# Performance work log

Hardware: AMD Instinct MI355X
Metric: run time of the kernel (lower is better)

Reference implementation:

```python
import jax, jax.numpy as jnp
import numpy as np
import math

S, E, D, H = 2048, 1024, 64, 16  # seq, embedding_dim (=D*H), per-head d_model, heads


def setup_inputs() -> dict:
    ks = jax.random.split(jax.random.key(0), 14)
    u = lambda k, sh: jax.random.uniform(k, sh, dtype=jnp.float32)
    n = lambda k, sh, s=0.02: s * jax.random.normal(k, sh, dtype=jnp.float32)
    return {
        "x": jax.random.normal(ks[0], (S, E), dtype=jnp.float32),
        # nn.Parameter(torch.rand(d_model, embedding_dim))
        "Wk": u(ks[1], (D, E)),
        "Wq": u(ks[2], (D, E)),
        "Wv": u(ks[3], (D, E)),
        # per-head Linear(d_model, d_model): weight [out,in]=[D,D], bias [D]
        "hWk": n(ks[4], (H, D, D)), "hbk": n(ks[5], (H, D)),
        "hWv": n(ks[6], (H, D, D)), "hbv": n(ks[7], (H, D)),
        "hWq": n(ks[8], (H, D, D)), "hbq": n(ks[9], (H, D)),
        # last_linear: Linear(D*H, D*H)
        "Wo": n(ks[10], (E, E)), "bo": n(ks[11], (E,)),
        # LayerNorm(D*H)
        "gamma": jnp.ones((E,), jnp.float32),
        "beta": jnp.zeros((E,), jnp.float32),
    }


def reference(x, Wk, Wq, Wv, hWk, hbk, hWv, hbv, hWq, hbq, Wo, bo, gamma, beta):
    # shared projections: [S, E] @ [E, D] -> [S, D]
    K = x @ Wk.T
    Q = x @ Wq.T
    V = x @ Wv.T
    # per-head linears (torch Linear: y = x @ W.T + b), vectorized over heads
    Kh = jnp.einsum('sd,hed->hse', K, hWk) + hbk[:, None, :]  # [H, S, D]
    Vh = jnp.einsum('sd,hed->hse', V, hWv) + hbv[:, None, :]
    Qh = jnp.einsum('sd,hed->hse', Q, hWq) + hbq[:, None, :]
    # scaled dot product attention; scale uses sqrt(d_model)
    scores = jnp.einsum('hqd,hkd->hqk', Qh, Kh) / math.sqrt(D)  # [H, S, S]
    attn = jax.nn.softmax(scores, axis=-1)
    O = jnp.einsum('hqk,hkd->hqd', attn, Vh)  # [H, S, D]
    # concat heads along feature dim (head order) -> [S, H*D]
    cat = jnp.transpose(O, (1, 0, 2)).reshape(S, H * D)
    out = cat @ Wo.T + bo
    # residual + LayerNorm (eps 1e-5)
    y = out + x
    mu = jnp.mean(y, axis=-1, keepdims=True)
    var = jnp.mean(jnp.square(y - mu), axis=-1, keepdims=True)
    return (y - mu) * jax.lax.rsqrt(var + 1e-5) * gamma + beta
```

## Files before the change

kernel.cpp:

```cpp
#include <hip/hip_runtime.h>
#include <math.h>

#define S 2048
#define E 1024
#define D 64
#define H 16

using f16 = _Float16;
typedef _Float16 v8h __attribute__((ext_vector_type(8)));
typedef _Float16 v4h __attribute__((ext_vector_type(4)));
typedef float v4f __attribute__((ext_vector_type(4)));

__device__ __forceinline__ void glds16(const f16* g, f16* l) {
    __builtin_amdgcn_global_load_lds(
        (const __attribute__((address_space(1))) void*)g,
        (__attribute__((address_space(3))) void*)l, 16, 0, 0);
}

__global__ void x_convert(const float* __restrict__ x, f16* __restrict__ Xh) {
    const size_t i = (size_t)blockIdx.x * 256 + threadIdx.x;
    v4f w = ((const v4f*)x)[i];
    v4h h = {(f16)w[0], (f16)w[1], (f16)w[2], (f16)w[3]};
    ((v4h*)Xh)[i] = h;
}
__global__ void wo_convert(const float* __restrict__ Wo, f16* __restrict__ WoB) {
    const size_t i = (size_t)blockIdx.x * 256 + threadIdx.x;
    v4f w = ((const v4f*)Wo)[i];
    v4h h = {(f16)w[0], (f16)w[1], (f16)w[2], (f16)w[3]};
    ((v4h*)WoB)[i] = h;
}

__global__ void wprep(const float* __restrict__ hWk, const float* __restrict__ hWq,
                      const float* __restrict__ hWv,
                      const float* __restrict__ Wk, const float* __restrict__ Wq,
                      const float* __restrict__ Wv,
                      f16* __restrict__ Wc) {
    const int th = blockIdx.x;
    const int type = th >> 4, h = th & 15;
    const int e0 = blockIdx.y * 64;
    const float* hW = ((type == 0) ? hWk : (type == 1) ? hWq : hWv) + (size_t)h * D * D;
    const float* W  = (type == 0) ? Wk : (type == 1) ? Wq : Wv;
    const int t = threadIdx.x;

    __shared__ f16 Ah[64][72];
    __shared__ f16 Bt[64][72];

    {
        const int r16 = t >> 4, c4 = (t & 15) * 4;
#pragma unroll
        for (int rep = 0; rep < 4; ++rep) {
            const int row = rep * 16 + r16;
            v4f a = *(const v4f*)&hW[(size_t)row * D + c4];
#pragma unroll
            for (int j = 0; j < 4; ++j) Ah[row][c4 + j] = (f16)a[j];
            v4f w = *(const v4f*)&W[(size_t)row * E + e0 + c4];
#pragma unroll
            for (int j = 0; j < 4; ++j) Bt[c4 + j][row] = (f16)w[j];
        }
    }
    __syncthreads();

    const int wave = t >> 6, lane = t & 63;
    const int quad = lane >> 4, l16 = lane & 15;
    v4f acc[4] = {{0,0,0,0},{0,0,0,0},{0,0,0,0},{0,0,0,0}};
#pragma unroll
    for (int ks = 0; ks < 2; ++ks) {
        v8h af = *(const v8h*)&Ah[wave * 16 + l16][ks * 32 + quad * 8];
#pragma unroll
        for (int nt = 0; nt < 4; ++nt) {
            v8h bf = *(const v8h*)&Bt[nt * 16 + l16][ks * 32 + quad * 8];
            acc[nt] = __builtin_amdgcn_mfma_f32_16x16x32_f16(af, bf, acc[nt], 0, 0, 0);
        }
    }
#pragma unroll
    for (int r = 0; r < 4; ++r) {
        const int e2 = wave * 16 + quad * 4 + r;
#pragma unroll
        for (int nt = 0; nt < 4; ++nt)
            Wc[((size_t)th * D + e2) * E + e0 + nt * 16 + l16] = (f16)acc[nt][r];
    }
}

__global__ __launch_bounds__(256) void qkv_gemm(
        const f16* __restrict__ Xh, const f16* __restrict__ Wc,
        const float* __restrict__ hbk, const float* __restrict__ hbq,
        const float* __restrict__ hbv,
        f16* __restrict__ Kh, f16* __restrict__ Qh, f16* __restrict__ Vh) {
    const int m0 = blockIdx.x * 128;
    const int n0 = blockIdx.y * 64;
    const int type = n0 >> 10, h = (n0 >> 6) & 15;
    const float* hb = ((type == 0) ? hbk : (type == 1) ? hbq : hbv) + h * D;
    f16* outp = (type == 0) ? Kh : (type == 1) ? Qh : Vh;

    const int t = threadIdx.x;
    const int wave = t >> 6, lane = t & 63;
    const int quad = lane >> 4, l16 = lane & 15;
    const int wm = wave >> 1, wn = wave & 1;

    __shared__ f16 As[128 * 64];
    __shared__ f16 Bs[64 * 64];

    v4f acc[4][2] = {};

    const int lrow8 = lane >> 3, lg = lane & 7;

    for (int k0 = 0; k0 < E; k0 += 64) {
        __syncthreads();
#pragma unroll
        for (int jj = 0; jj < 4; ++jj) {
            const int j = wave * 4 + jj;
            const int row = j * 8 + lrow8;
            const int g = lg ^ (row & 7);
            glds16(Xh + (size_t)(m0 + row) * E + k0 + g * 8, &As[j * 512]);
        }
#pragma unroll
        for (int jj = 0; jj < 2; ++jj) {
            const int j = wave * 2 + jj;
            const int row = j * 8 + lrow8;
            const int g = lg ^ (row & 7);
            glds16(Wc + (size_t)(n0 + row) * E + k0 + g * 8, &Bs[j * 512]);
        }
        __syncthreads();

#pragma unroll
        for (int ks = 0; ks < 2; ++ks) {
            v8h a[4], b[2];
#pragma unroll
            for (int mt = 0; mt < 4; ++mt) {
                const int row = wm * 64 + mt * 16 + l16;
                a[mt] = *(const v8h*)&As[row * 64 + (((ks * 4 + quad) ^ (row & 7)) * 8)];
            }
#pragma unroll
            for (int nt = 0; nt < 2; ++nt) {
                const int row = wn * 32 + nt * 16 + l16;
                b[nt] = *(const v8h*)&Bs[row * 64 + (((ks * 4 + quad) ^ (row & 7)) * 8)];
            }
#pragma unroll
            for (int mt = 0; mt < 4; ++mt)
#pragma unroll
                for (int nt = 0; nt < 2; ++nt)
                    acc[mt][nt] = __builtin_amdgcn_mfma_f32_16x16x32_f16(a[mt], b[nt], acc[mt][nt], 0, 0, 0);
        }
    }

#pragma unroll
    for (int mt = 0; mt < 4; ++mt)
#pragma unroll
        for (int r = 0; r < 4; ++r) {
            const int s = m0 + wm * 64 + mt * 16 + quad * 4 + r;
#pragma unroll
            for (int nt = 0; nt < 2; ++nt) {
                const int d = wn * 32 + nt * 16 + l16;
                outp[((size_t)h * S + s) * D + d] = (f16)(acc[mt][nt][r] + hb[d]);
            }
        }
}

__global__ void v_transpose(const f16* __restrict__ Vh, f16* __restrict__ VhT) {
    const int h = blockIdx.x;
    const int s0 = blockIdx.y * 64;
    const int t = threadIdx.x;

    __shared__ f16 T[64][66];

    {
        const int r = t >> 2, c = (t & 3) * 16;
        v8h a = *(const v8h*)(Vh + ((size_t)h * S + s0 + r) * D + c);
        v8h b = *(const v8h*)(Vh + ((size_t)h * S + s0 + r) * D + c + 8);
#pragma unroll
        for (int j = 0; j < 8; ++j) { T[r][c + j] = a[j]; T[r][c + 8 + j] = b[j]; }
    }
    __syncthreads();
    {
        const int d = t >> 2, sc = (t & 3) * 16;
        v8h a, b;
#pragma unroll
        for (int j = 0; j < 8; ++j) { a[j] = T[sc + j][d]; b[j] = T[sc + 8 + j][d]; }
        f16* o = VhT + ((size_t)h * D + d) * S + s0 + sc;
        *(v8h*)o = a;
        *(v8h*)(o + 8) = b;
    }
}

#define TK2 64
#define NSPLIT 2
#define KSPAN (S / NSPLIT)
#define ITERS (KSPAN / TK2)
#define APAD 72

__global__ __launch_bounds__(256) void attn_mfma(
        const f16* __restrict__ Qh, const f16* __restrict__ Kh,
        const f16* __restrict__ VhT, f16* __restrict__ Opart,
        float* __restrict__ ml) {
    const int h = blockIdx.y;
    const int q0 = blockIdx.x * 64;
    const int sp = blockIdx.z;
    const int t = threadIdx.x;
    const int wave = t >> 6, lane = t & 63;
    const int quad = lane >> 4, l16 = lane & 15;

    __shared__ f16 Kt[TK2][APAD];
    __shared__ f16 Vt[D][APAD];
    __shared__ f16 Pt[4][16][APAD];
    __shared__ f16 Ot[64][APAD];

    const int qrow = q0 + wave * 16 + l16;
    v8h qf[2];
    {
        const v8h* qp = (const v8h*)(Qh + ((size_t)h * S + qrow) * D);
        qf[0] = qp[quad];
        qf[1] = qp[quad + 4];
    }

    v4f oc[4] = {};
    float m_run = -INFINITY, l_run = 0.f;
    const float scale = 0.125f * 1.44269504f;

    const int sr = t >> 2, scc = (t & 3) * 16;
    const int kb = sp * KSPAN;

    v8h kA, kB, vA, vB;
    {
        const f16* kg = Kh + ((size_t)h * S + kb + sr) * D + scc;
        kA = *(const v8h*)kg; kB = *(const v8h*)(kg + 8);
        const f16* vg = VhT + ((size_t)h * D + sr) * S + kb + scc;
        vA = *(const v8h*)vg; vB = *(const v8h*)(vg + 8);
    }

    for (int it = 0; it < ITERS; ++it) {
        __syncthreads();
        *(v8h*)&Kt[sr][scc] = kA;  *(v8h*)&Kt[sr][scc + 8] = kB;
        *(v8h*)&Vt[sr][scc] = vA;  *(v8h*)&Vt[sr][scc + 8] = vB;
        __syncthreads();

        if (it + 1 < ITERS) {
            const int nb = kb + (it + 1) * TK2;
            const f16* kg = Kh + ((size_t)h * S + nb + sr) * D + scc;
            kA = *(const v8h*)kg; kB = *(const v8h*)(kg + 8);
            const f16* vg = VhT + ((size_t)h * D + sr) * S + nb + scc;
            vA = *(const v8h*)vg; vB = *(const v8h*)(vg + 8);
        }

        v4f sc[4] = {};
#pragma unroll
        for (int ks = 0; ks < 2; ++ks) {
#pragma unroll
            for (int mt = 0; mt < 4; ++mt) {
                v8h kf = *(const v8h*)&Kt[mt * 16 + l16][ks * 32 + quad * 8];
                sc[mt] = __builtin_amdgcn_mfma_f32_16x16x32_f16(kf, qf[ks], sc[mt], 0, 0, 0);
            }
        }

        float v = sc[0][0];
#pragma unroll
        for (int mt = 0; mt < 4; ++mt)
#pragma unroll
            for (int r = 0; r < 4; ++r) v = fmaxf(v, sc[mt][r]);
        v = fmaxf(v, __shfl_xor(v, 16));
        v = fmaxf(v, __shfl_xor(v, 32));
        v *= scale;
        const float mnew = fmaxf(m_run, v);
        const float alpha = exp2f(m_run - mnew);
        m_run = mnew;

        float tsum = 0.f;
#pragma unroll
        for (int mt = 0; mt < 4; ++mt) {
            v4h ph;
#pragma unroll
            for (int r = 0; r < 4; ++r) {
                const float p = exp2f(fmaf(sc[mt][r], scale, -mnew));
                tsum += p;
                ph[r] = (f16)p;
            }
            *(v4h*)&Pt[wave][l16][mt * 16 + quad * 4] = ph;
        }
        tsum += __shfl_xor(tsum, 16);
        tsum += __shfl_xor(tsum, 32);
        l_run = l_run * alpha + tsum;
#pragma unroll
        for (int mt = 0; mt < 4; ++mt) oc[mt] *= alpha;

#pragma unroll
        for (int ks = 0; ks < 2; ++ks) {
            v8h pf = *(const v8h*)&Pt[wave][l16][ks * 32 + quad * 8];
#pragma unroll
            for (int mt = 0; mt < 4; ++mt) {
                v8h vf = *(const v8h*)&Vt[mt * 16 + l16][ks * 32 + quad * 8];
                oc[mt] = __builtin_amdgcn_mfma_f32_16x16x32_f16(vf, pf, oc[mt], 0, 0, 0);
            }
        }
    }

    const float invl = 1.f / l_run;
#pragma unroll
    for (int mt = 0; mt < 4; ++mt) {
        v4h oh;
#pragma unroll
        for (int r = 0; r < 4; ++r) oh[r] = (f16)(oc[mt][r] * invl);
        *(v4h*)&Ot[wave * 16 + l16][mt * 16 + quad * 4] = oh;
    }
    if (quad == 0) {
        float* mlp = ml + (((size_t)sp * H + h) * S + qrow) * 2;
        mlp[0] = m_run;
        mlp[1] = l_run;
    }
    __syncthreads();
    {
        const int q = t >> 2, dg = (t & 3) * 16;
        v8h o0 = *(const v8h*)&Ot[q][dg];
        v8h o1 = *(const v8h*)&Ot[q][dg + 8];
        f16* dst = Opart + (((size_t)sp * H + h) * S + q0 + q) * D + dg;
        *(v8h*)dst = o0;
        *(v8h*)(dst + 8) = o1;
    }
}

__global__ void attn_combine(const f16* __restrict__ Opart,
                             const float* __restrict__ ml,
                             f16* __restrict__ cat) {
    const int q = blockIdx.x;
    const int t = threadIdx.x;
#pragma unroll
    for (int i = 0; i < 4; ++i) {
        const int idx = i * 256 + t;
        const int h = idx >> 6, d = idx & 63;
        const size_t b0 = ((size_t)0 * H + h) * S + q;
        const size_t b1 = ((size_t)1 * H + h) * S + q;
        const float m0 = ml[b0 * 2], l0 = ml[b0 * 2 + 1];
        const float m1 = ml[b1 * 2], l1 = ml[b1 * 2 + 1];
        const float M = fmaxf(m0, m1);
        const float a0 = exp2f(m0 - M) * l0;
        const float a1 = exp2f(m1 - M) * l1;
        const float inv = 1.f / (a0 + a1);
        const float o = (a0 * (float)Opart[b0 * D + d] + a1 * (float)Opart[b1 * D + d]) * inv;
        cat[(size_t)q * E + h * D + d] = (f16)o;
    }
}

__global__ __launch_bounds__(256) void gemm_y(
        const f16* __restrict__ cat, const f16* __restrict__ WoB,
        const float* __restrict__ bo, const float* __restrict__ x,
        float* __restrict__ y) {
    const int m0 = blockIdx.x * 64;
    const int n0 = blockIdx.y * 64;
    const int t = threadIdx.x;
    const int wave = t >> 6, lane = t & 63;
    const int quad = lane >> 4, l16 = lane & 15;
    const int wm = wave >> 1, wn = wave & 1;

    __shared__ f16 As[64 * 64];
    __shared__ f16 Bs[64 * 64];

    v4f acc[2][2] = {};
    const int lrow8 = lane >> 3, lg = lane & 7;

    for (int k0 = 0; k0 < E; k0 += 64) {
        __syncthreads();
#pragma unroll
        for (int jj = 0; jj < 2; ++jj) {
            const int j = wave * 2 + jj;
            const int row = j * 8 + lrow8;
            const int g = lg ^ (row & 7);
            glds16(cat + (size_t)(m0 + row) * E + k0 + g * 8, &As[j * 512]);
            glds16(WoB + (size_t)(n0 + row) * E + k0 + g * 8, &Bs[j * 512]);
        }
        __syncthreads();

#pragma unroll
        for (int ks = 0; ks < 2; ++ks) {
            v8h a[2], b[2];
#pragma unroll
            for (int mt = 0; mt < 2; ++mt) {
                const int row = wm * 32 + mt * 16 + l16;
                a[mt] = *(const v8h*)&As[row * 64 + (((ks * 4 + quad) ^ (row & 7)) * 8)];
            }
#pragma unroll
            for (int nt = 0; nt < 2; ++nt) {
                const int row = wn * 32 + nt * 16 + l16;
                b[nt] = *(const v8h*)&Bs[row * 64 + (((ks * 4 + quad) ^ (row & 7)) * 8)];
            }
#pragma unroll
            for (int mt = 0; mt < 2; ++mt)
#pragma unroll
                for (int nt = 0; nt < 2; ++nt)
                    acc[mt][nt] = __builtin_amdgcn_mfma_f32_16x16x32_f16(a[mt], b[nt], acc[mt][nt], 0, 0, 0);
        }
    }

#pragma unroll
    for (int mt = 0; mt < 2; ++mt)
#pragma unroll
        for (int r = 0; r < 4; ++r) {
            const int m = m0 + wm * 32 + mt * 16 + quad * 4 + r;
#pragma unroll
            for (int nt = 0; nt < 2; ++nt) {
                const int e = n0 + wn * 32 + nt * 16 + l16;
                y[(size_t)m * E + e] = acc[mt][nt][r] + bo[e] + x[(size_t)m * E + e];
            }
        }
}

__global__ void ln(const float* __restrict__ y,
                   const float* __restrict__ gamma,
                   const float* __restrict__ beta,
                   float* __restrict__ out) {
    const int s = blockIdx.x;
    const int t = threadIdx.x;
    __shared__ float red[256];

    v4f yv = *(const v4f*)(y + (size_t)s * E + t * 4);
    float lsum = yv[0] + yv[1] + yv[2] + yv[3];
    red[t] = lsum;
    __syncthreads();
    for (int w = 128; w > 0; w >>= 1) {
        if (t < w) red[t] += red[t + w];
        __syncthreads();
    }
    const float mu = red[0] * (1.f / E);
    __syncthreads();

    float lv = 0.f;
#pragma unroll
    for (int i = 0; i < 4; ++i) { float dd = yv[i] - mu; lv += dd * dd; }
    red[t] = lv;
    __syncthreads();
    for (int w = 128; w > 0; w >>= 1) {
        if (t < w) red[t] += red[t + w];
        __syncthreads();
    }
    const float rstd = rsqrtf(red[0] * (1.f / E) + 1e-5f);

    v4f o;
#pragma unroll
    for (int i = 0; i < 4; ++i) {
        const int e = t * 4 + i;
        o[i] = (yv[i] - mu) * rstd * gamma[e] + beta[e];
    }
    *(v4f*)(out + (size_t)s * E + t * 4) = o;
}

extern "C" void kernel_launch(void* const* d_in, const int* in_sizes, int n_in,
                              void* d_out, int out_size, void* d_ws, size_t ws_size,
                              hipStream_t stream) {
    const float* x     = (const float*)d_in[0];
    const float* Wk    = (const float*)d_in[1];
    const float* Wq    = (const float*)d_in[2];
    const float* Wv    = (const float*)d_in[3];
    const float* hWk   = (const float*)d_in[4];
    const float* hbk   = (const float*)d_in[5];
    const float* hWv   = (const float*)d_in[6];
    const float* hbv   = (const float*)d_in[7];
    const float* hWq   = (const float*)d_in[8];
    const float* hbq   = (const float*)d_in[9];
    const float* Wo    = (const float*)d_in[10];
    const float* bo    = (const float*)d_in[11];
    const float* gamma = (const float*)d_in[12];
    const float* beta  = (const float*)d_in[13];
    float* out = (float*)d_out;

    char* base = (char*)d_ws;
    const size_t MB = 1u << 20;
    f16*   Xh    = (f16*)(base);
    f16*   Wc    = (f16*)(base + 4 * MB);
    f16*   Kh    = (f16*)(base + 12 * MB);
    f16*   Qh    = (f16*)(base + 16 * MB);
    f16*   Vh    = (f16*)(base + 20 * MB);
    f16*   VhT   = (f16*)(base);
    f16*   Opart = (f16*)(base + 4 * MB);
    f16*   cat   = (f16*)(base + 24 * MB);
    f16*   WoB   = (f16*)(base + 28 * MB);
    float* ml    = (float*)(base + 30 * MB);
    float* y     = (float*)(base);

    x_convert<<<(S * E / 4) / 256, 256, 0, stream>>>(x, Xh);
    wo_convert<<<(E * E / 4) / 256, 256, 0, stream>>>(Wo, WoB);
    wprep<<<dim3(3 * H, E / 64), 256, 0, stream>>>(hWk, hWq, hWv, Wk, Wq, Wv, Wc);
    qkv_gemm<<<dim3(S / 128, 3 * H * D / 64), 256, 0, stream>>>(Xh, Wc, hbk, hbq, hbv,
                                                                Kh, Qh, Vh);
    v_transpose<<<dim3(H, S / 64), 256, 0, stream>>>(Vh, VhT);
    attn_mfma<<<dim3(S / 64, H, NSPLIT), 256, 0, stream>>>(Qh, Kh, VhT, Opart, ml);
    attn_combine<<<S, 256, 0, stream>>>(Opart, ml, cat);
    gemm_y<<<dim3(S / 64, E / 64), 256, 0, stream>>>(cat, WoB, bo, x, y);
    ln<<<S, 256, 0, stream>>>(y, gamma, beta, out);
}
```

Baseline: 179.5 us.

## Rework attention: direct-to-LDS swizzled K/V loads, 4-way split, MFMA row sum

The attention kernel now loads K and V^T tiles straight into swizzled LDS with global_load_lds instead of staging them through registers. The key dimension is split 4 ways instead of 2, and launch bounds are raised to 5 blocks per CU. The softmax row sum is computed by an extra MFMA against a row of ones appended to V, and the exponentials use the hardware exp2 intrinsic with packed f16 conversion. The two conversion kernels are merged into one and workspace buffers are rearranged. The cost is the loss of register prefetch overlap and more partial outputs for the combine step to merge.

```diff
diff --git a/kernel.cpp b/kernel.cpp
--- a/kernel.cpp
+++ b/kernel.cpp
@@ -9,7 +9,10 @@
 using f16 = _Float16;
 typedef _Float16 v8h __attribute__((ext_vector_type(8)));
 typedef _Float16 v4h __attribute__((ext_vector_type(4)));
+typedef _Float16 v2h __attribute__((ext_vector_type(2)));
 typedef float v4f __attribute__((ext_vector_type(4)));
+
+__device__ __forceinline__ float fexp2(float x) { return __builtin_amdgcn_exp2f(x); }
 
 __device__ __forceinline__ void glds16(const f16* g, f16* l) {
     __builtin_amdgcn_global_load_lds(
@@ -17,17 +20,20 @@
         (__attribute__((address_space(3))) void*)l, 16, 0, 0);
 }
 
-__global__ void x_convert(const float* __restrict__ x, f16* __restrict__ Xh) {
+__global__ void convert_all(const float* __restrict__ x, const float* __restrict__ Wo,
+                            f16* __restrict__ Xh, f16* __restrict__ WoB) {
     const size_t i = (size_t)blockIdx.x * 256 + threadIdx.x;
-    v4f w = ((const v4f*)x)[i];
-    v4h h = {(f16)w[0], (f16)w[1], (f16)w[2], (f16)w[3]};
-    ((v4h*)Xh)[i] = h;
-}
-__global__ void wo_convert(const float* __restrict__ Wo, f16* __restrict__ WoB) {
-    const size_t i = (size_t)blockIdx.x * 256 + threadIdx.x;
-    v4f w = ((const v4f*)Wo)[i];
-    v4h h = {(f16)w[0], (f16)w[1], (f16)w[2], (f16)w[3]};
-    ((v4h*)WoB)[i] = h;
+    const size_t NX = (size_t)S * E / 4;
+    if (i < NX) {
+        v4f w = ((const v4f*)x)[i];
+        v4h h = {(f16)w[0], (f16)w[1], (f16)w[2], (f16)w[3]};
+        ((v4h*)Xh)[i] = h;
+    } else {
+        const size_t j = i - NX;
+        v4f w = ((const v4f*)Wo)[j];
+        v4h h = {(f16)w[0], (f16)w[1], (f16)w[2], (f16)w[3]};
+        ((v4h*)WoB)[j] = h;
+    }
 }
 
 __global__ void wprep(const float* __restrict__ hWk, const float* __restrict__ hWq,
@@ -101,7 +107,6 @@
     __shared__ f16 Bs[64 * 64];
 
     v4f acc[4][2] = {};
-
     const int lrow8 = lane >> 3, lg = lane & 7;
 
     for (int k0 = 0; k0 < E; k0 += 64) {
@@ -182,13 +187,12 @@
     }
 }
 
-#define TK2 64
-#define NSPLIT 2
+#define NSPLIT 4
 #define KSPAN (S / NSPLIT)
-#define ITERS (KSPAN / TK2)
-#define APAD 72
-
-__global__ __launch_bounds__(256) void attn_mfma(
+#define ITERS (KSPAN / 64)
+#define PPAD 72
+
+__global__ __launch_bounds__(256, 5) void attn_mfma(
         const f16* __restrict__ Qh, const f16* __restrict__ Kh,
         const f16* __restrict__ VhT, f16* __restrict__ Opart,
         float* __restrict__ ml) {
@@ -199,10 +203,14 @@
     const int wave = t >> 6, lane = t & 63;
     const int quad = lane >> 4, l16 = lane & 15;
 
-    __shared__ f16 Kt[TK2][APAD];
-    __shared__ f16 Vt[D][APAD];
-    __shared__ f16 Pt[4][16][APAD];
-    __shared__ f16 Ot[64][APAD];
+    __shared__ f16 Kt[64 * 64];
+    __shared__ f16 Vt[80 * 64];
+    __shared__ union { f16 P[4][16][PPAD]; f16 O[64][PPAD]; } PO;
+
+    {
+        v4h one = {(f16)1, (f16)1, (f16)1, (f16)1};
+        *(v4h*)&Vt[64 * 64 + t * 4] = one;
+    }
 
     const int qrow = q0 + wave * 16 + l16;
     v8h qf[2];
@@ -212,44 +220,34 @@
         qf[1] = qp[quad + 4];
     }
 
-    v4f oc[4] = {};
-    float m_run = -INFINITY, l_run = 0.f;
+    v4f oc[5] = {};
+    float m_run = -INFINITY;
     const float scale = 0.125f * 1.44269504f;
-
-    const int sr = t >> 2, scc = (t & 3) * 16;
     const int kb = sp * KSPAN;
-
-    v8h kA, kB, vA, vB;
-    {
-        const f16* kg = Kh + ((size_t)h * S + kb + sr) * D + scc;
-        kA = *(const v8h*)kg; kB = *(const v8h*)(kg + 8);
-        const f16* vg = VhT + ((size_t)h * D + sr) * S + kb + scc;
-        vA = *(const v8h*)vg; vB = *(const v8h*)(vg + 8);
-    }
+    const int srow = lane >> 3, sg = lane & 7;
 
     for (int it = 0; it < ITERS; ++it) {
         __syncthreads();
-        *(v8h*)&Kt[sr][scc] = kA;  *(v8h*)&Kt[sr][scc + 8] = kB;
-        *(v8h*)&Vt[sr][scc] = vA;  *(v8h*)&Vt[sr][scc + 8] = vB;
-        __syncthreads();
-
-        if (it + 1 < ITERS) {
-            const int nb = kb + (it + 1) * TK2;
-            const f16* kg = Kh + ((size_t)h * S + nb + sr) * D + scc;
-            kA = *(const v8h*)kg; kB = *(const v8h*)(kg + 8);
-            const f16* vg = VhT + ((size_t)h * D + sr) * S + nb + scc;
-            vA = *(const v8h*)vg; vB = *(const v8h*)(vg + 8);
-        }
+#pragma unroll
+        for (int half = 0; half < 2; ++half) {
+            const int row = wave * 16 + half * 8 + srow;
+            const int g = sg ^ (row & 7);
+            glds16(Kh + ((size_t)h * S + kb + it * 64 + row) * D + g * 8,
+                   &Kt[(wave * 16 + half * 8) * 64]);
+            glds16(VhT + ((size_t)h * D + row) * S + kb + it * 64 + g * 8,
+                   &Vt[(wave * 16 + half * 8) * 64]);
+        }
+        __syncthreads();
 
         v4f sc[4] = {};
 #pragma unroll
-        for (int ks = 0; ks < 2; ++ks) {
+        for (int ks = 0; ks < 2; ++ks)
 #pragma unroll
             for (int mt = 0; mt < 4; ++mt) {
-                v8h kf = *(const v8h*)&Kt[mt * 16 + l16][ks * 32 + quad * 8];
+                const int key = mt * 16 + l16;
+                v8h kf = *(const v8h*)&Kt[key * 64 + (((ks * 4 + quad) ^ (key & 7)) * 8)];
                 sc[mt] = __builtin_amdgcn_mfma_f32_16x16x32_f16(kf, qf[ks], sc[mt], 0, 0, 0);
             }
-        }
 
         float v = sc[0][0];
 #pragma unroll
@@ -260,56 +258,55 @@
         v = fmaxf(v, __shfl_xor(v, 32));
         v *= scale;
         const float mnew = fmaxf(m_run, v);
-        const float alpha = exp2f(m_run - mnew);
+        const float alpha = fexp2(m_run - mnew);
         m_run = mnew;
-
-        float tsum = 0.f;
+#pragma unroll
+        for (int i = 0; i < 5; ++i) oc[i] *= alpha;
+
 #pragma unroll
         for (int mt = 0; mt < 4; ++mt) {
-            v4h ph;
-#pragma unroll
-            for (int r = 0; r < 4; ++r) {
-                const float p = exp2f(fmaf(sc[mt][r], scale, -mnew));
-                tsum += p;
-                ph[r] = (f16)p;
-            }
-            *(v4h*)&Pt[wave][l16][mt * 16 + quad * 4] = ph;
-        }
-        tsum += __shfl_xor(tsum, 16);
-        tsum += __shfl_xor(tsum, 32);
-        l_run = l_run * alpha + tsum;
-#pragma unroll
-        for (int mt = 0; mt < 4; ++mt) oc[mt] *= alpha;
+            const float p0 = fexp2(fmaf(sc[mt][0], scale, -mnew));
+            const float p1 = fexp2(fmaf(sc[mt][1], scale, -mnew));
+            const float p2 = fexp2(fmaf(sc[mt][2], scale, -mnew));
+            const float p3 = fexp2(fmaf(sc[mt][3], scale, -mnew));
+            auto lo = __builtin_amdgcn_cvt_pkrtz(p0, p1);
+            auto hi = __builtin_amdgcn_cvt_pkrtz(p2, p3);
+            v4h ph; ph[0] = lo[0]; ph[1] = lo[1]; ph[2] = hi[0]; ph[3] = hi[1];
+            *(v4h*)&PO.P[wave][l16][mt * 16 + quad * 4] = ph;
+        }
 
 #pragma unroll
         for (int ks = 0; ks < 2; ++ks) {
-            v8h pf = *(const v8h*)&Pt[wave][l16][ks * 32 + quad * 8];
-#pragma unroll
-            for (int mt = 0; mt < 4; ++mt) {
-                v8h vf = *(const v8h*)&Vt[mt * 16 + l16][ks * 32 + quad * 8];
+            v8h pf = *(const v8h*)&PO.P[wave][l16][ks * 32 + quad * 8];
+#pragma unroll
+            for (int mt = 0; mt < 5; ++mt) {
+                const int dr = mt * 16 + l16;
+                v8h vf = *(const v8h*)&Vt[dr * 64 + (((ks * 4 + quad) ^ (dr & 7)) * 8)];
                 oc[mt] = __builtin_amdgcn_mfma_f32_16x16x32_f16(vf, pf, oc[mt], 0, 0, 0);
             }
         }
     }
 
-    const float invl = 1.f / l_run;
+    const float l = oc[4][0];
+    const float invl = 1.f / l;
+    __syncthreads();
 #pragma unroll
     for (int mt = 0; mt < 4; ++mt) {
-        v4h oh;
-#pragma unroll
-        for (int r = 0; r < 4; ++r) oh[r] = (f16)(oc[mt][r] * invl);
-        *(v4h*)&Ot[wave * 16 + l16][mt * 16 + quad * 4] = oh;
+        auto lo = __builtin_amdgcn_cvt_pkrtz(oc[mt][0] * invl, oc[mt][1] * invl);
+        auto hi = __builtin_amdgcn_cvt_pkrtz(oc[mt][2] * invl, oc[mt][3] * invl);
+        v4h oh; oh[0] = lo[0]; oh[1] = lo[1]; oh[2] = hi[0]; oh[3] = hi[1];
+        *(v4h*)&PO.O[wave * 16 + l16][mt * 16 + quad * 4] = oh;
     }
     if (quad == 0) {
         float* mlp = ml + (((size_t)sp * H + h) * S + qrow) * 2;
         mlp[0] = m_run;
-        mlp[1] = l_run;
+        mlp[1] = l;
     }
     __syncthreads();
     {
         const int q = t >> 2, dg = (t & 3) * 16;
-        v8h o0 = *(const v8h*)&Ot[q][dg];
-        v8h o1 = *(const v8h*)&Ot[q][dg + 8];
+        v8h o0 = *(const v8h*)&PO.O[q][dg];
+        v8h o1 = *(const v8h*)&PO.O[q][dg + 8];
         f16* dst = Opart + (((size_t)sp * H + h) * S + q0 + q) * D + dg;
         *(v8h*)dst = o0;
         *(v8h*)(dst + 8) = o1;
@@ -325,16 +322,22 @@
     for (int i = 0; i < 4; ++i) {
         const int idx = i * 256 + t;
         const int h = idx >> 6, d = idx & 63;
-        const size_t b0 = ((size_t)0 * H + h) * S + q;
-        const size_t b1 = ((size_t)1 * H + h) * S + q;
-        const float m0 = ml[b0 * 2], l0 = ml[b0 * 2 + 1];
-        const float m1 = ml[b1 * 2], l1 = ml[b1 * 2 + 1];
-        const float M = fmaxf(m0, m1);
-        const float a0 = exp2f(m0 - M) * l0;
-        const float a1 = exp2f(m1 - M) * l1;
-        const float inv = 1.f / (a0 + a1);
-        const float o = (a0 * (float)Opart[b0 * D + d] + a1 * (float)Opart[b1 * D + d]) * inv;
-        cat[(size_t)q * E + h * D + d] = (f16)o;
+        float m[NSPLIT], lv[NSPLIT];
+        float M = -INFINITY;
+#pragma unroll
+        for (int sp = 0; sp < NSPLIT; ++sp) {
+            const float* mlp = ml + (((size_t)sp * H + h) * S + q) * 2;
+            m[sp] = mlp[0]; lv[sp] = mlp[1];
+            M = fmaxf(M, m[sp]);
+        }
+        float asum = 0.f, o = 0.f;
+#pragma unroll
+        for (int sp = 0; sp < NSPLIT; ++sp) {
+            const float a = fexp2(m[sp] - M) * lv[sp];
+            asum += a;
+            o += a * (float)Opart[(((size_t)sp * H + h) * S + q) * D + d];
+        }
+        cat[(size_t)q * E + h * D + d] = (f16)(o / asum);
     }
 }
 
@@ -410,8 +413,7 @@
     __shared__ float red[256];
 
     v4f yv = *(const v4f*)(y + (size_t)s * E + t * 4);
-    float lsum = yv[0] + yv[1] + yv[2] + yv[3];
-    red[t] = lsum;
+    red[t] = yv[0] + yv[1] + yv[2] + yv[3];
     __syncthreads();
     for (int w = 128; w > 0; w >>= 1) {
         if (t < w) red[t] += red[t + w];
@@ -461,20 +463,19 @@
 
     char* base = (char*)d_ws;
     const size_t MB = 1u << 20;
-    f16*   Xh    = (f16*)(base);
-    f16*   Wc    = (f16*)(base + 4 * MB);
-    f16*   Kh    = (f16*)(base + 12 * MB);
-    f16*   Qh    = (f16*)(base + 16 * MB);
-    f16*   Vh    = (f16*)(base + 20 * MB);
-    f16*   VhT   = (f16*)(base);
-    f16*   Opart = (f16*)(base + 4 * MB);
-    f16*   cat   = (f16*)(base + 24 * MB);
-    f16*   WoB   = (f16*)(base + 28 * MB);
-    float* ml    = (float*)(base + 30 * MB);
-    float* y     = (float*)(base);
-
-    x_convert<<<(S * E / 4) / 256, 256, 0, stream>>>(x, Xh);
-    wo_convert<<<(E * E / 4) / 256, 256, 0, stream>>>(Wo, WoB);
+    f16*   Kh    = (f16*)(base);
+    f16*   Qh    = (f16*)(base + 4 * MB);
+    f16*   VhT   = (f16*)(base + 8 * MB);
+    f16*   Opart = (f16*)(base + 12 * MB);
+    float* ml    = (float*)(base + 28 * MB);
+    f16*   WoB   = (f16*)(base + 29 * MB);
+    f16*   Xh    = (f16*)(base + 12 * MB);
+    f16*   Wc    = (f16*)(base + 16 * MB);
+    f16*   Vh    = (f16*)(base + 22 * MB);
+    f16*   cat   = (f16*)(base);
+    float* y     = (float*)(base + 4 * MB);
+
+    convert_all<<<3072, 256, 0, stream>>>(x, Wo, Xh, WoB);
     wprep<<<dim3(3 * H, E / 64), 256, 0, stream>>>(hWk, hWq, hWv, Wk, Wq, Wv, Wc);
     qkv_gemm<<<dim3(S / 128, 3 * H * D / 64), 256, 0, stream>>>(Xh, Wc, hbk, hbq, hbv,
                                                                 Kh, Qh, Vh);
```

Result: faster. 170.4 us (-5.1%).
